# Kernel tuning notes

Hardware: AMD Instinct MI355X
Metric: run time of the kernel (lower is better)

Reference implementation:

```python
import jax, jax.numpy as jnp
import numpy as np

D_MODEL = 2048
NUM_HEADS = 32
NUM_KV_HEADS = 8
D_K = D_MODEL // NUM_HEADS  # 64
GROUPS = NUM_HEADS // NUM_KV_HEADS  # 4
KV_DIM = NUM_KV_HEADS * D_K  # 512


def setup_inputs() -> dict:
    key = jax.random.key(0)
    ks = jax.random.split(key, 9)
    s = 0.02
    return {
        "x": jax.random.normal(ks[0], (2, 2048, D_MODEL), dtype=jnp.float32),
        "Wq": jax.random.normal(ks[1], (D_MODEL, D_MODEL), dtype=jnp.float32) * s,
        "bq": jnp.zeros((D_MODEL,), dtype=jnp.float32),
        "Wk": jax.random.normal(ks[2], (D_MODEL, KV_DIM), dtype=jnp.float32) * s,
        "bk": jnp.zeros((KV_DIM,), dtype=jnp.float32),
        "Wv": jax.random.normal(ks[3], (D_MODEL, KV_DIM), dtype=jnp.float32) * s,
        "bv": jnp.zeros((KV_DIM,), dtype=jnp.float32),
        "Wo": jax.random.normal(ks[4], (D_MODEL, D_MODEL), dtype=jnp.float32) * s,
        "bo": jnp.zeros((D_MODEL,), dtype=jnp.float32),
    }


def reference(x, Wq, bq, Wk, bk, Wv, bv, Wo, bo):
    B, S, _ = x.shape
    # projections
    Q = (x @ Wq + bq).reshape(B, S, NUM_HEADS, D_K).transpose(0, 2, 1, 3)      # [B,H,S,dk]
    K = (x @ Wk + bk).reshape(B, S, NUM_KV_HEADS, D_K).transpose(0, 2, 1, 3)   # [B,Hkv,S,dk]
    V = (x @ Wv + bv).reshape(B, S, NUM_KV_HEADS, D_K).transpose(0, 2, 1, 3)
    # repeat_interleave KV heads to match query heads
    K = jnp.repeat(K, GROUPS, axis=1)  # [B,H,S,dk]
    V = jnp.repeat(V, GROUPS, axis=1)
    scale = 1.0 / jnp.sqrt(jnp.asarray(D_K, dtype=x.dtype))
    scores = jnp.einsum("bhqd,bhkd->bhqk", Q, K) * scale  # [B,H,S,S]
    attn = jax.nn.softmax(scores, axis=-1)
    out = jnp.einsum("bhqk,bhkd->bhqd", attn, V)           # [B,H,S,dk]
    out = out.transpose(0, 2, 1, 3).reshape(B, S, D_MODEL)
    return out @ Wo + bo
```

## Files before the change

kernel.cpp:

```cpp
#include <hip/hip_runtime.h>
#include <hip/hip_bf16.h>
#include <stdint.h>

typedef __bf16 bf16;
typedef __bf16 bf16x8 __attribute__((ext_vector_type(8)));
typedef float  f32x2  __attribute__((ext_vector_type(2)));
typedef float  f32x4  __attribute__((ext_vector_type(4)));
typedef float  f32x16 __attribute__((ext_vector_type(16)));

#define D_MODEL 2048
#define KV_DIM  512
#define SEQ     2048
#define BATCH   2
#define MTOT    (BATCH*SEQ)
#define QKV_N   3072
#define QSCALE  (0.125f*1.44269504088896f)

#if __has_builtin(__builtin_amdgcn_exp2f)
#define EXP2(x) __builtin_amdgcn_exp2f(x)
#else
#define EXP2(x) exp2f(x)
#endif

__global__ __launch_bounds__(256) void cvt_f32_bf16(const float* __restrict__ in,
                                                    bf16* __restrict__ out, int n) {
  int i = (blockIdx.x * 256 + threadIdx.x) * 4;
  if (i < n) {
    float4 v = *reinterpret_cast<const float4*>(in + i);
    bf16 o[4] = {(bf16)v.x, (bf16)v.y, (bf16)v.z, (bf16)v.w};
    *reinterpret_cast<uint64_t*>(out + i) = *reinterpret_cast<const uint64_t*>(o);
  }
}

__global__ __launch_bounds__(256) void transpose_all(
    const float* __restrict__ Wq, const float* __restrict__ Wk,
    const float* __restrict__ Wv, const float* __restrict__ Wo,
    bf16* __restrict__ Wall, bf16* __restrict__ Wot) {
  const int z = blockIdx.z;
  const float* W; bf16* dst; int N;
  if (z == 0)      { W = Wq; dst = Wall;                          N = 2048; }
  else if (z == 1) { W = Wk; dst = Wall + (size_t)2048 * 2048;    N = 512;  }
  else if (z == 2) { W = Wv; dst = Wall + (size_t)2560 * 2048;    N = 512;  }
  else             { W = Wo; dst = Wot;                           N = 2048; }
  const int n0 = blockIdx.x * 64, k0 = blockIdx.y * 64;
  if (n0 >= N) return;
  __shared__ float tile[64][65];
  const int tx = threadIdx.x & 63;
  const int ty = threadIdx.x >> 6;
  #pragma unroll
  for (int i = ty; i < 64; i += 4)
    tile[i][tx] = W[(size_t)(k0 + i) * N + n0 + tx];
  __syncthreads();
  #pragma unroll
  for (int i = ty; i < 64; i += 4)
    dst[(size_t)(n0 + i) * 2048 + k0 + tx] = (bf16)tile[tx][i];
}

__global__ __launch_bounds__(256) void transpose_v(const bf16* __restrict__ QKV,
                                                   bf16* __restrict__ Vtg) {
  __shared__ bf16 t[64][72];
  const int st = blockIdx.x;
  const int bk = blockIdx.y;
  const int b = bk >> 3, kvh = bk & 7;
  const int tid = threadIdx.x;
  const int r = tid >> 2, c = (tid & 3) * 16;
  const bf16* src = QKV + (size_t)(b * SEQ + st * 64 + r) * QKV_N + 2560 + kvh * 64 + c;
  *(bf16x8*)&t[r][c]     = *(const bf16x8*)src;
  *(bf16x8*)&t[r][c + 8] = *(const bf16x8*)(src + 8);
  __syncthreads();
  bf16 tmp[16];
  #pragma unroll
  for (int j = 0; j < 16; ++j) tmp[j] = t[c + j][r];
  bf16* dst = Vtg + (size_t)(bk * 64 + r) * SEQ + st * 64 + c;
  *(bf16x8*)dst       = *(const bf16x8*)tmp;
  *(bf16x8*)(dst + 8) = *(const bf16x8*)(tmp + 8);
}

__device__ __forceinline__ void gload_lds16(const bf16* g, bf16* l) {
  __builtin_amdgcn_global_load_lds(
      (const __attribute__((address_space(1))) uint32_t*)g,
      (__attribute__((address_space(3))) uint32_t*)l, 16, 0, 0);
}

__device__ __forceinline__ uint32_t pk2(float a, float b) {
  union { bf16 h[2]; uint32_t u; } v;
  v.h[0] = (bf16)a; v.h[1] = (bf16)b;
  return v.u;
}

template<int NF, int OUT_BF16>
__global__ __launch_bounds__(512, 2) void gemm256(
    const bf16* __restrict__ A, const bf16* __restrict__ Bt,
    const float* __restrict__ b0, const float* __restrict__ b1,
    const float* __restrict__ b2, int sp1, int sp2, int nscale, float scale,
    void* __restrict__ Cout, int N, int K)
{
  __shared__ bf16 As[2][256 * 64];
  __shared__ bf16 Bs[2][NF * 64 * 64];

  const int tid = threadIdx.x, lane = tid & 63;
  const int wid = tid >> 6;
  const int wr = wid >> 1, wc = wid & 1;
  const int l31 = lane & 31, hi2 = lane >> 5;
  const int rx = l31 & 7;

  const int bid = blockIdx.y * 16 + blockIdx.x;
  const int swz = (bid & 7) * 32 + (bid >> 3);
  const int m0 = (swz >> 4) * 256, n0 = (swz & 15) * (NF * 64);

  const int srow = tid >> 3;
  const int schk = (tid & 7) ^ (srow & 7);
  const bf16* aSrc = A  + (size_t)(m0 + srow) * K + schk * 8;
  const bf16* bSrc = Bt + (size_t)(n0 + srow) * K + schk * 8;
  const size_t rstep = (size_t)64 * K;

  f32x16 acc[2][NF] = {};

  const int NT = K / 64;

#define G256_STAGE(T, BUF)                                            \
  {                                                                   \
    const bf16* a_ = aSrc + (T) * 64;                                 \
    _Pragma("unroll")                                                 \
    for (int j = 0; j < 4; ++j)                                       \
      gload_lds16(a_ + j * rstep, &As[BUF][j * 4096 + tid * 8]);      \
    const bf16* b_ = bSrc + (T) * 64;                                 \
    _Pragma("unroll")                                                 \
    for (int j = 0; j < NF; ++j)                                      \
      gload_lds16(b_ + j * rstep, &Bs[BUF][j * 4096 + tid * 8]);      \
  }

#define G256_WAITL()                                                  \
  if constexpr (NF == 3) asm volatile("s_waitcnt vmcnt(7)" ::: "memory"); \
  else                   asm volatile("s_waitcnt vmcnt(6)" ::: "memory");

#define G256_BODY(BUF)                                                \
  {                                                                   \
    _Pragma("unroll")                                                 \
    for (int ks = 0; ks < 4; ++ks) {                                  \
      bf16x8 af[2], bfv[NF];                                          \
      _Pragma("unroll")                                               \
      for (int m = 0; m < 2; ++m)                                     \
        af[m] = *(const bf16x8*)&As[BUF][(wr * 64 + m * 32 + l31) * 64 \
                                         + (((ks * 2 + hi2) ^ rx) * 8)]; \
      _Pragma("unroll")                                               \
      for (int n = 0; n < NF; ++n)                                    \
        bfv[n] = *(const bf16x8*)&Bs[BUF][(wc * (NF * 32) + n * 32 + l31) * 64 \
                                          + (((ks * 2 + hi2) ^ rx) * 8)]; \
      __builtin_amdgcn_s_setprio(1);                                  \
      _Pragma("unroll")                                               \
      for (int m = 0; m < 2; ++m)                                     \
        _Pragma("unroll")                                             \
        for (int n = 0; n < NF; ++n)                                  \
          acc[m][n] = __builtin_amdgcn_mfma_f32_32x32x16_bf16(        \
              af[m], bfv[n], acc[m][n], 0, 0, 0);                     \
      __builtin_amdgcn_s_setprio(0);                                  \
    }                                                                 \
  }

  G256_STAGE(0, 0)
  G256_STAGE(1, 1)
  G256_WAITL()
  __builtin_amdgcn_sched_barrier(0);
  __builtin_amdgcn_s_barrier();
  __builtin_amdgcn_sched_barrier(0);

  for (int t = 0; t < NT; t += 2) {
    #pragma unroll
    for (int u = 0; u < 2; ++u) {
      G256_BODY(u)
      __builtin_amdgcn_sched_barrier(0);
      __builtin_amdgcn_s_barrier();
      __builtin_amdgcn_sched_barrier(0);
      const int tt = t + u;
      if (tt < NT - 2) {
        G256_STAGE(tt + 2, u)
        G256_WAITL()
      } else {
        asm volatile("s_waitcnt vmcnt(0)" ::: "memory");
      }
      __builtin_amdgcn_sched_barrier(0);
      __builtin_amdgcn_s_barrier();
      __builtin_amdgcn_sched_barrier(0);
    }
  }

#undef G256_STAGE
#undef G256_WAITL
#undef G256_BODY

  const int cb = n0 + wc * (NF * 32) + l31;
  #pragma unroll
  for (int n = 0; n < NF; ++n) {
    const int col = cb + n * 32;
    float bv;
    if (col < sp1)      bv = b0[col];
    else if (col < sp2) bv = b1[col - sp1];
    else                bv = b2[col - sp2];
    const float scl = (col < nscale) ? scale : 1.0f;
    #pragma unroll
    for (int m = 0; m < 2; ++m) {
      const int rb = m0 + wr * 64 + m * 32 + 4 * hi2;
      #pragma unroll
      for (int r = 0; r < 16; ++r) {
        const int row = rb + (r & 3) + 8 * (r >> 2);
        const float v = (acc[m][n][r] + bv) * scl;
        if (OUT_BF16) ((bf16*)Cout)[(size_t)row * N + col] = (bf16)v;
        else          ((float*)Cout)[(size_t)row * N + col] = v;
      }
    }
  }
}

__global__ __launch_bounds__(256) void attn_kernel(
    const bf16* __restrict__ QKV, const bf16* __restrict__ Vtg, bf16* __restrict__ ctx)
{
  __shared__ bf16 smem[4][64 * 64];

  const int tid = threadIdx.x, lane = tid & 63, wid = tid >> 6;
  const int l31 = lane & 31, hi = lane >> 5;
  const int qt = blockIdx.x & 15;
  const int bh = blockIdx.x >> 4;
  const int h = bh & 31, b = bh >> 5, kvh = h >> 2;

  const bf16* gK = QKV + (size_t)b * SEQ * QKV_N + 2048 + kvh * 64;
  const bf16* gV = Vtg + (size_t)(b * 8 + kvh) * 64 * SEQ;

  const int sr  = lane >> 3;
  const int scn = (lane & 7) ^ sr;

  bf16x8 qf[4];
  {
    const bf16* qp = QKV + (size_t)(b * SEQ + qt * 128 + wid * 32 + l31) * QKV_N + h * 64 + hi * 8;
    #pragma unroll
    for (int kt = 0; kt < 4; ++kt) qf[kt] = *(const bf16x8*)(qp + kt * 16);
  }

  bf16x8 onesv;
  #pragma unroll
  for (int j = 0; j < 8; ++j) onesv[j] = (bf16)1.0f;

  f32x16 o0 = {}, o1 = {};
  f32x16 lacc = {};

  const int row0 = (wid * 2 + 0) * 8 + sr;
  const int row1 = (wid * 2 + 1) * 8 + sr;
  const bf16* pK0 = gK + (size_t)row0 * QKV_N + scn * 8;
  const bf16* pK1 = gK + (size_t)row1 * QKV_N + scn * 8;
  const bf16* pV0 = gV + (size_t)row0 * SEQ + scn * 8;
  const bf16* pV1 = gV + (size_t)row1 * SEQ + scn * 8;

  gload_lds16(pK0, &smem[0][(wid * 2 + 0) * 512]);
  gload_lds16(pK1, &smem[0][(wid * 2 + 1) * 512]);
  gload_lds16(pV0, &smem[2][(wid * 2 + 0) * 512]);
  gload_lds16(pV1, &smem[2][(wid * 2 + 1) * 512]);
  pK0 += (size_t)64 * QKV_N; pK1 += (size_t)64 * QKV_N; pV0 += 64; pV1 += 64;
  __syncthreads();

  const int rx = l31 & 7;

  for (int it = 0; it < 32; ++it) {
    const int cur = it & 1;
    if (it < 31) {
      gload_lds16(pK0, &smem[cur ^ 1][(wid * 2 + 0) * 512]);
      gload_lds16(pK1, &smem[cur ^ 1][(wid * 2 + 1) * 512]);
      gload_lds16(pV0, &smem[2 + (cur ^ 1)][(wid * 2 + 0) * 512]);
      gload_lds16(pV1, &smem[2 + (cur ^ 1)][(wid * 2 + 1) * 512]);
      pK0 += (size_t)64 * QKV_N; pK1 += (size_t)64 * QKV_N; pV0 += 64; pV1 += 64;
    }
    const bf16* Kb = smem[cur];
    const bf16* Vb = smem[2 + cur];

    bf16x8 kf[8];
    #pragma unroll
    for (int kt = 0; kt < 4; ++kt) {
      const int ck = hi + 2 * kt;
      kf[kt]     = *(const bf16x8*)(Kb + (size_t)l31 * 64        + ((ck ^ rx) * 8));
      kf[kt + 4] = *(const bf16x8*)(Kb + (size_t)(32 + l31) * 64 + ((ck ^ rx) * 8));
    }
    f32x16 s0v = {}, s1v = {};
    __builtin_amdgcn_s_setprio(1);
    #pragma unroll
    for (int kt = 0; kt < 4; ++kt) {
      s0v = __builtin_amdgcn_mfma_f32_32x32x16_bf16(kf[kt],     qf[kt], s0v, 0, 0, 0);
      s1v = __builtin_amdgcn_mfma_f32_32x32x16_bf16(kf[kt + 4], qf[kt], s1v, 0, 0, 0);
    }
    __builtin_amdgcn_s_setprio(0);

    bf16x8 vf[8];
    #pragma unroll
    for (int s = 0; s < 4; ++s) {
      const int ck = hi + 2 * s;
      vf[s]     = *(const bf16x8*)(Vb + (size_t)l31 * 64        + ((ck ^ rx) * 8));
      vf[s + 4] = *(const bf16x8*)(Vb + (size_t)(32 + l31) * 64 + ((ck ^ rx) * 8));
    }

    #pragma unroll
    for (int r = 0; r < 16; ++r) { s0v[r] = EXP2(s0v[r]); s1v[r] = EXP2(s1v[r]); }

    #pragma unroll
    for (int s = 0; s < 4; ++s) {
      const f32x16& sv = (s < 2) ? s0v : s1v;
      const int rb = (s & 1) * 8;
      uint32_t Aw = pk2(sv[rb + 0], sv[rb + 1]);
      uint32_t Bw = pk2(sv[rb + 2], sv[rb + 3]);
      uint32_t Cw = pk2(sv[rb + 4], sv[rb + 5]);
      uint32_t Dw = pk2(sv[rb + 6], sv[rb + 7]);
      union { uint32_t w[4]; bf16x8 v; } pf;
#if __has_builtin(__builtin_amdgcn_permlane32_swap)
      auto rA = __builtin_amdgcn_permlane32_swap(Aw, Cw, false, false);
      auto rB = __builtin_amdgcn_permlane32_swap(Bw, Dw, false, false);
      pf.w[0] = rA[0]; pf.w[1] = rB[0]; pf.w[2] = rA[1]; pf.w[3] = rB[1];
#else
      uint32_t U = hi ? Aw : Cw;
      uint32_t W = hi ? Bw : Dw;
      uint32_t pU = (uint32_t)__shfl_xor((int)U, 32);
      uint32_t pW = (uint32_t)__shfl_xor((int)W, 32);
      pf.w[0] = hi ? pU : Aw;
      pf.w[1] = hi ? pW : Bw;
      pf.w[2] = hi ? Cw : pU;
      pf.w[3] = hi ? Dw : pW;
#endif
      __builtin_amdgcn_s_setprio(1);
      o0 = __builtin_amdgcn_mfma_f32_32x32x16_bf16(vf[s],     pf.v, o0, 0, 0, 0);
      o1 = __builtin_amdgcn_mfma_f32_32x32x16_bf16(vf[s + 4], pf.v, o1, 0, 0, 0);
      lacc = __builtin_amdgcn_mfma_f32_32x32x16_bf16(onesv,   pf.v, lacc, 0, 0, 0);
      __builtin_amdgcn_s_setprio(0);
    }
    __syncthreads();
  }

  const float inv = 1.0f / lacc[0];
  o0 *= inv; o1 *= inv;

  uint32_t* ot = (uint32_t*)((bf16*)smem + wid * 2304);
  #pragma unroll
  for (int r = 0; r < 16; r += 2) {
    const int d = (r & 3) + 8 * (r >> 2) + 4 * hi;
    ot[l31 * 36 + (d >> 1)]        = pk2(o0[r], o0[r + 1]);
    ot[l31 * 36 + ((32 + d) >> 1)] = pk2(o1[r], o1[r + 1]);
  }
  __syncthreads();
  {
    const int q2 = lane >> 1, hf = lane & 1;
    const bf16* src = (const bf16*)smem + wid * 2304 + q2 * 72 + hf * 32;
    bf16* dst = ctx + (size_t)(b * SEQ + qt * 128 + wid * 32 + q2) * D_MODEL + h * 64 + hf * 32;
    #pragma unroll
    for (int k = 0; k < 4; ++k)
      *(bf16x8*)(dst + k * 8) = *(const bf16x8*)(src + k * 8);
  }
}

extern "C" void kernel_launch(void* const* d_in, const int* in_sizes, int n_in,
                              void* d_out, int out_size, void* d_ws, size_t ws_size,
                              hipStream_t stream) {
  const float* x  = (const float*)d_in[0];
  const float* Wq = (const float*)d_in[1];
  const float* bq = (const float*)d_in[2];
  const float* Wk = (const float*)d_in[3];
  const float* bk = (const float*)d_in[4];
  const float* Wv = (const float*)d_in[5];
  const float* bv = (const float*)d_in[6];
  const float* Wo = (const float*)d_in[7];
  const float* bo = (const float*)d_in[8];
  float* out = (float*)d_out;

  char* ws = (char*)d_ws;
  size_t off = 0;
  bf16* xb   = (bf16*)(ws + off); off += (size_t)MTOT * D_MODEL * 2;
  bf16* Wall = (bf16*)(ws + off); off += (size_t)QKV_N * D_MODEL * 2;
  bf16* Wot  = (bf16*)(ws + off); off += (size_t)D_MODEL * D_MODEL * 2;
  bf16* QKV  = (bf16*)(ws + off); off += (size_t)MTOT * QKV_N * 2;
  bf16* ctx  = (bf16*)(ws + off); off += (size_t)MTOT * D_MODEL * 2;
  bf16* Vtg  = (bf16*)(ws + off); off += (size_t)16 * 64 * SEQ * 2;

  {
    int n = MTOT * D_MODEL;
    cvt_f32_bf16<<<n / 4 / 256, 256, 0, stream>>>(x, xb, n);
  }
  transpose_all<<<dim3(32, 32, 4), 256, 0, stream>>>(Wq, Wk, Wv, Wo, Wall, Wot);

  gemm256<3, 1><<<dim3(16, 16), 512, 0, stream>>>(
      xb, Wall, bq, bk, bv, 2048, 2560, 2048, QSCALE, QKV, QKV_N, D_MODEL);

  transpose_v<<<dim3(SEQ / 64, 16), 256, 0, stream>>>(QKV, Vtg);

  attn_kernel<<<dim3((SEQ / 128) * BATCH * 32), 256, 0, stream>>>(QKV, Vtg, ctx);

  gemm256<2, 0><<<dim3(16, 16), 512, 0, stream>>>(
      ctx, Wot, bo, bo, bo, 2048, 2048, 0, 1.0f, out, D_MODEL, D_MODEL);
}
```

Before: 235.0 us.

## Process two 32-row query sets per warp to reuse K/V tiles in attention

The attention kernel now gives each warp 64 query rows instead of 32, so one block covers 256 queries and the grid shrinks by half. Each K/V tile loaded into shared memory and registers is reused for twice as many query rows, halving global K/V traffic and LDS reads per query. In exchange, register pressure rises (extra accumulators and score tiles), so launch_bounds(256,2) is added. The grid drops to 512 blocks, and the fallback path without permlane32_swap is removed.

```diff
diff --git a/kernel.cpp b/kernel.cpp
--- a/kernel.cpp
+++ b/kernel.cpp
@@ -212,15 +212,15 @@
   }
 }
 
-__global__ __launch_bounds__(256) void attn_kernel(
+__global__ __launch_bounds__(256, 2) void attn_kernel(
     const bf16* __restrict__ QKV, const bf16* __restrict__ Vtg, bf16* __restrict__ ctx)
 {
   __shared__ bf16 smem[4][64 * 64];
 
   const int tid = threadIdx.x, lane = tid & 63, wid = tid >> 6;
   const int l31 = lane & 31, hi = lane >> 5;
-  const int qt = blockIdx.x & 15;
-  const int bh = blockIdx.x >> 4;
+  const int qt = blockIdx.x & 7;
+  const int bh = blockIdx.x >> 3;
   const int h = bh & 31, b = bh >> 5, kvh = h >> 2;
 
   const bf16* gK = QKV + (size_t)b * SEQ * QKV_N + 2048 + kvh * 64;
@@ -229,19 +229,22 @@
   const int sr  = lane >> 3;
   const int scn = (lane & 7) ^ sr;
 
-  bf16x8 qf[4];
+  bf16x8 qf[4], qf2[4];
   {
-    const bf16* qp = QKV + (size_t)(b * SEQ + qt * 128 + wid * 32 + l31) * QKV_N + h * 64 + hi * 8;
-    #pragma unroll
-    for (int kt = 0; kt < 4; ++kt) qf[kt] = *(const bf16x8*)(qp + kt * 16);
+    const bf16* qp = QKV + (size_t)(b * SEQ + qt * 256 + wid * 64 + l31) * QKV_N + h * 64 + hi * 8;
+    #pragma unroll
+    for (int kt = 0; kt < 4; ++kt) qf[kt]  = *(const bf16x8*)(qp + kt * 16);
+    const bf16* qp2 = qp + (size_t)32 * QKV_N;
+    #pragma unroll
+    for (int kt = 0; kt < 4; ++kt) qf2[kt] = *(const bf16x8*)(qp2 + kt * 16);
   }
 
   bf16x8 onesv;
   #pragma unroll
   for (int j = 0; j < 8; ++j) onesv[j] = (bf16)1.0f;
 
-  f32x16 o0 = {}, o1 = {};
-  f32x16 lacc = {};
+  f32x16 o0 = {}, o1 = {}, o2 = {}, o3 = {};
+  f32x16 lacc = {}, lacc2 = {};
 
   const int row0 = (wid * 2 + 0) * 8 + sr;
   const int row1 = (wid * 2 + 1) * 8 + sr;
@@ -258,6 +261,26 @@
   __syncthreads();
 
   const int rx = l31 & 7;
+
+#define PV_SET(SA, SB, OA, OB, LC)                                        \
+    _Pragma("unroll")                                                     \
+    for (int s = 0; s < 4; ++s) {                                         \
+      const f32x16& sv = (s < 2) ? SA : SB;                               \
+      const int rb = (s & 1) * 8;                                         \
+      uint32_t Aw = pk2(sv[rb + 0], sv[rb + 1]);                          \
+      uint32_t Bw = pk2(sv[rb + 2], sv[rb + 3]);                          \
+      uint32_t Cw = pk2(sv[rb + 4], sv[rb + 5]);                          \
+      uint32_t Dw = pk2(sv[rb + 6], sv[rb + 7]);                          \
+      union { uint32_t w[4]; bf16x8 v; } pf;                              \
+      auto rA = __builtin_amdgcn_permlane32_swap(Aw, Cw, false, false);   \
+      auto rB = __builtin_amdgcn_permlane32_swap(Bw, Dw, false, false);   \
+      pf.w[0] = rA[0]; pf.w[1] = rB[0]; pf.w[2] = rA[1]; pf.w[3] = rB[1]; \
+      __builtin_amdgcn_s_setprio(1);                                      \
+      OA = __builtin_amdgcn_mfma_f32_32x32x16_bf16(vf[s],     pf.v, OA, 0, 0, 0); \
+      OB = __builtin_amdgcn_mfma_f32_32x32x16_bf16(vf[s + 4], pf.v, OB, 0, 0, 0); \
+      LC = __builtin_amdgcn_mfma_f32_32x32x16_bf16(onesv,     pf.v, LC, 0, 0, 0); \
+      __builtin_amdgcn_s_setprio(0);                                      \
+    }
 
   for (int it = 0; it < 32; ++it) {
     const int cur = it & 1;
@@ -278,12 +301,14 @@
       kf[kt]     = *(const bf16x8*)(Kb + (size_t)l31 * 64        + ((ck ^ rx) * 8));
       kf[kt + 4] = *(const bf16x8*)(Kb + (size_t)(32 + l31) * 64 + ((ck ^ rx) * 8));
     }
-    f32x16 s0v = {}, s1v = {};
+    f32x16 s0v = {}, s1v = {}, s2v = {}, s3v = {};
     __builtin_amdgcn_s_setprio(1);
     #pragma unroll
     for (int kt = 0; kt < 4; ++kt) {
-      s0v = __builtin_amdgcn_mfma_f32_32x32x16_bf16(kf[kt],     qf[kt], s0v, 0, 0, 0);
-      s1v = __builtin_amdgcn_mfma_f32_32x32x16_bf16(kf[kt + 4], qf[kt], s1v, 0, 0, 0);
+      s0v = __builtin_amdgcn_mfma_f32_32x32x16_bf16(kf[kt],     qf[kt],  s0v, 0, 0, 0);
+      s1v = __builtin_amdgcn_mfma_f32_32x32x16_bf16(kf[kt + 4], qf[kt],  s1v, 0, 0, 0);
+      s2v = __builtin_amdgcn_mfma_f32_32x32x16_bf16(kf[kt],     qf2[kt], s2v, 0, 0, 0);
+      s3v = __builtin_amdgcn_mfma_f32_32x32x16_bf16(kf[kt + 4], qf2[kt], s3v, 0, 0, 0);
     }
     __builtin_amdgcn_s_setprio(0);
 
@@ -296,59 +321,44 @@
     }
 
     #pragma unroll
-    for (int r = 0; r < 16; ++r) { s0v[r] = EXP2(s0v[r]); s1v[r] = EXP2(s1v[r]); }
-
-    #pragma unroll
-    for (int s = 0; s < 4; ++s) {
-      const f32x16& sv = (s < 2) ? s0v : s1v;
-      const int rb = (s & 1) * 8;
-      uint32_t Aw = pk2(sv[rb + 0], sv[rb + 1]);
-      uint32_t Bw = pk2(sv[rb + 2], sv[rb + 3]);
-      uint32_t Cw = pk2(sv[rb + 4], sv[rb + 5]);
-      uint32_t Dw = pk2(sv[rb + 6], sv[rb + 7]);
-      union { uint32_t w[4]; bf16x8 v; } pf;
-#if __has_builtin(__builtin_amdgcn_permlane32_swap)
-      auto rA = __builtin_amdgcn_permlane32_swap(Aw, Cw, false, false);
-      auto rB = __builtin_amdgcn_permlane32_swap(Bw, Dw, false, false);
-      pf.w[0] = rA[0]; pf.w[1] = rB[0]; pf.w[2] = rA[1]; pf.w[3] = rB[1];
-#else
-      uint32_t U = hi ? Aw : Cw;
-      uint32_t W = hi ? Bw : Dw;
-      uint32_t pU = (uint32_t)__shfl_xor((int)U, 32);
-      uint32_t pW = (uint32_t)__shfl_xor((int)W, 32);
-      pf.w[0] = hi ? pU : Aw;
-      pf.w[1] = hi ? pW : Bw;
-      pf.w[2] = hi ? Cw : pU;
-      pf.w[3] = hi ? Dw : pW;
-#endif
-      __builtin_amdgcn_s_setprio(1);
-      o0 = __builtin_amdgcn_mfma_f32_32x32x16_bf16(vf[s],     pf.v, o0, 0, 0, 0);
-      o1 = __builtin_amdgcn_mfma_f32_32x32x16_bf16(vf[s + 4], pf.v, o1, 0, 0, 0);
-      lacc = __builtin_amdgcn_mfma_f32_32x32x16_bf16(onesv,   pf.v, lacc, 0, 0, 0);
-      __builtin_amdgcn_s_setprio(0);
-    }
+    for (int r = 0; r < 16; ++r) {
+      s0v[r] = EXP2(s0v[r]); s1v[r] = EXP2(s1v[r]);
+      s2v[r] = EXP2(s2v[r]); s3v[r] = EXP2(s3v[r]);
+    }
+
+    PV_SET(s0v, s1v, o0, o1, lacc)
+    PV_SET(s2v, s3v, o2, o3, lacc2)
     __syncthreads();
   }
-
-  const float inv = 1.0f / lacc[0];
-  o0 *= inv; o1 *= inv;
-
-  uint32_t* ot = (uint32_t*)((bf16*)smem + wid * 2304);
-  #pragma unroll
-  for (int r = 0; r < 16; r += 2) {
-    const int d = (r & 3) + 8 * (r >> 2) + 4 * hi;
-    ot[l31 * 36 + (d >> 1)]        = pk2(o0[r], o0[r + 1]);
-    ot[l31 * 36 + ((32 + d) >> 1)] = pk2(o1[r], o1[r + 1]);
-  }
-  __syncthreads();
-  {
-    const int q2 = lane >> 1, hf = lane & 1;
-    const bf16* src = (const bf16*)smem + wid * 2304 + q2 * 72 + hf * 32;
-    bf16* dst = ctx + (size_t)(b * SEQ + qt * 128 + wid * 32 + q2) * D_MODEL + h * 64 + hf * 32;
-    #pragma unroll
-    for (int k = 0; k < 4; ++k)
-      *(bf16x8*)(dst + k * 8) = *(const bf16x8*)(src + k * 8);
-  }
+#undef PV_SET
+
+#define WRITE_SET(OA, OB, LC, QOFF)                                        \
+  {                                                                        \
+    const float inv = 1.0f / LC[0];                                        \
+    OA *= inv; OB *= inv;                                                  \
+    uint32_t* ot = (uint32_t*)((bf16*)smem + wid * 2304);                  \
+    _Pragma("unroll")                                                      \
+    for (int r = 0; r < 16; r += 2) {                                      \
+      const int d = (r & 3) + 8 * (r >> 2) + 4 * hi;                       \
+      ot[l31 * 36 + (d >> 1)]        = pk2(OA[r], OA[r + 1]);              \
+      ot[l31 * 36 + ((32 + d) >> 1)] = pk2(OB[r], OB[r + 1]);              \
+    }                                                                      \
+    __syncthreads();                                                       \
+    {                                                                      \
+      const int q2 = lane >> 1, hf = lane & 1;                             \
+      const bf16* src = (const bf16*)smem + wid * 2304 + q2 * 72 + hf * 32;\
+      bf16* dst = ctx + (size_t)(b * SEQ + qt * 256 + wid * 64 + (QOFF) + q2) * D_MODEL \
+                      + h * 64 + hf * 32;                                  \
+      _Pragma("unroll")                                                    \
+      for (int k = 0; k < 4; ++k)                                          \
+        *(bf16x8*)(dst + k * 8) = *(const bf16x8*)(src + k * 8);           \
+    }                                                                      \
+    __syncthreads();                                                       \
+  }
+
+  WRITE_SET(o0, o1, lacc, 0)
+  WRITE_SET(o2, o3, lacc2, 32)
+#undef WRITE_SET
 }
 
 extern "C" void kernel_launch(void* const* d_in, const int* in_sizes, int n_in,
@@ -385,7 +395,7 @@
 
   transpose_v<<<dim3(SEQ / 64, 16), 256, 0, stream>>>(QKV, Vtg);
 
-  attn_kernel<<<dim3((SEQ / 128) * BATCH * 32), 256, 0, stream>>>(QKV, Vtg, ctx);
+  attn_kernel<<<dim3((SEQ / 256) * BATCH * 32), 256, 0, stream>>>(QKV, Vtg, ctx);
 
   gemm256<2, 0><<<dim3(16, 16), 512, 0, stream>>>(
       ctx, Wot, bo, bo, bo, 2048, 2048, 0, 1.0f, out, D_MODEL, D_MODEL);
```

Measured after the change: 219.1 us. 1.07x faster.
